# Performance work log

Hardware: AMD Instinct MI355X
Metric: run time of the kernel (lower is better)

Reference implementation:

```python
import jax, jax.numpy as jnp
import numpy as np

SCALE = 2
GROUPS = 4


def setup_inputs() -> dict:
    key = jax.random.key(0)
    k1, k2 = jax.random.split(key, 2)
    B, C, H, W = 8, 256, 96, 96
    out_ch = 2 * GROUPS * SCALE ** 2  # 32
    x = jax.random.normal(k1, (B, C, H, W), dtype=jnp.float32)
    # offset conv: normal_init(std=0.001), bias=0
    w = jax.random.normal(k2, (out_ch, C), dtype=jnp.float32) * 0.001
    b = jnp.zeros((out_ch,), dtype=jnp.float32)
    return {"x": x, "w": w, "b": b}


def _grid_sample_bilinear_border(x, grid):
    """x: [N,C,H,W]; grid: [N,Ho,Wo,2] with (x,y) in [-1,1]; align_corners=False,
    padding_mode='border' (coords clamped to [0, size-1] before interpolation)."""
    N, C, H, W = x.shape
    Ho, Wo = grid.shape[1], grid.shape[2]
    gx = (grid[..., 0] + 1.0) * (W * 0.5) - 0.5
    gy = (grid[..., 1] + 1.0) * (H * 0.5) - 0.5
    gx = jnp.clip(gx, 0.0, W - 1.0)
    gy = jnp.clip(gy, 0.0, H - 1.0)
    x0 = jnp.floor(gx)
    y0 = jnp.floor(gy)
    wx = (gx - x0).reshape(N, 1, Ho * Wo)
    wy = (gy - y0).reshape(N, 1, Ho * Wo)
    x0i = x0.astype(jnp.int32)
    y0i = y0.astype(jnp.int32)
    x1i = jnp.minimum(x0i + 1, W - 1)
    y1i = jnp.minimum(y0i + 1, H - 1)
    xf = x.reshape(N, C, H * W)

    def gather(yi, xi):
        idx = (yi * W + xi).reshape(N, 1, Ho * Wo)
        return jnp.take_along_axis(xf, idx, axis=2)  # [N,C,Ho*Wo]

    v00 = gather(y0i, x0i)
    v01 = gather(y0i, x1i)
    v10 = gather(y1i, x0i)
    v11 = gather(y1i, x1i)
    out = (v00 * (1.0 - wx) * (1.0 - wy) + v01 * wx * (1.0 - wy)
           + v10 * (1.0 - wx) * wy + v11 * wx * wy)
    return out.reshape(N, C, Ho, Wo)


def reference(x, w, b):
    B, C, H, W = x.shape
    r, g = SCALE, GROUPS
    # 1x1 conv producing per-pixel offsets
    off = jnp.einsum('bchw,oc->bohw', x, w) + b[None, :, None, None]  # [B,32,H,W]
    Co = off.shape[1] // (r * r)  # 2*groups = 8
    # pixel_shuffle(r): out[b,c,h*r+i,w*r+j] = in[b, c*r*r + i*r + j, h, w]
    off = off.reshape(B, Co, r, r, H, W).transpose(0, 1, 4, 2, 5, 3)
    off = off.reshape(B, Co, H * r, W * r)
    off = jnp.tanh(off)
    Hs, Ws = H * r, W * r
    xr = x.reshape(B * g, C // g, H, W)
    off_field = off.reshape(B * g, 2, Hs, Ws).transpose(0, 2, 3, 1)  # [B*g,Hs,Ws,2]
    ry = jnp.linspace(-1.0 + 1.0 / Hs, 1.0 - 1.0 / Hs, Hs, dtype=jnp.float32)
    rx = jnp.linspace(-1.0 + 1.0 / Ws, 1.0 - 1.0 / Ws, Ws, dtype=jnp.float32)
    gy, gx = jnp.meshgrid(ry, rx, indexing='ij')
    base = jnp.stack([gx, gy], axis=-1)[None]  # [1,Hs,Ws,2]
    grid = base + off_field * 0.125
    out = _grid_sample_bilinear_border(xr, grid)
    return out.reshape(B, C, Hs, Ws)
```

## Files before the change

### kernel.cpp

```cpp
#include <hip/hip_runtime.h>

#define Cc  256
#define Hh  96
#define Ww  96
#define HW  (Hh*Ww)
#define OC  32
#define HS  192
#define WSS 192
#define PLANE (HS*WSS)
#define WT_FLOATS (Cc*OC)

__global__ __launch_bounds__(256) void transpose_w_kernel(
    const float* __restrict__ w, float* __restrict__ wt)
{
    const int l = blockIdx.x * 256 + threadIdx.x;
    const int o = l >> 8, c = l & 255;
    wt[c * OC + o] = w[l];
}

__global__ __launch_bounds__(256) void conv_offset_kernel(
    const float* __restrict__ x, const float* __restrict__ wt,
    const float* __restrict__ bias, float* __restrict__ grid_buf)
{
    __shared__ float lds[Cc * OC];
    const int tid   = threadIdx.x;
    const int pix   = tid & 63;
    const int slice = __builtin_amdgcn_readfirstlane(threadIdx.x >> 6);

    const int p  = blockIdx.x * 64 + pix;
    const int b  = p / HW;
    const int hw = p - b * HW;
    const float* xp = x + (size_t)b * Cc * HW + (size_t)(slice * 64) * HW + hw;
    const float* wp = wt + slice * (64 * OC);

    float acc[OC];
    #pragma unroll
    for (int o = 0; o < OC; ++o) acc[o] = 0.0f;

    #pragma unroll 4
    for (int c = 0; c < 64; ++c) {
        float xv = xp[(size_t)c * HW];
        const float4* w4 = (const float4*)&wp[c * OC];
        #pragma unroll
        for (int o4 = 0; o4 < 8; ++o4) {
            float4 wv = w4[o4];
            acc[4*o4+0] = fmaf(wv.x, xv, acc[4*o4+0]);
            acc[4*o4+1] = fmaf(wv.y, xv, acc[4*o4+1]);
            acc[4*o4+2] = fmaf(wv.z, xv, acc[4*o4+2]);
            acc[4*o4+3] = fmaf(wv.w, xv, acc[4*o4+3]);
        }
    }

    #pragma unroll
    for (int o = 0; o < OC; ++o) lds[(o * 4 + slice) * 64 + pix] = acc[o];
    __syncthreads();

    const int h  = hw / Ww;
    const int ww = hw - h * Ww;
    const int obase = slice * 8;
    #pragma unroll
    for (int oo = 0; oo < 8; ++oo) {
        const int o = obase + oo;
        float s = lds[(o * 4 + 0) * 64 + pix]
                + lds[(o * 4 + 1) * 64 + pix]
                + lds[(o * 4 + 2) * 64 + pix]
                + lds[(o * 4 + 3) * 64 + pix] + bias[o];
        const int co  = o >> 2;
        const int rem = o & 3;
        const int i   = rem >> 1;
        const int j   = rem & 1;
        const int gr  = co >> 1;
        const int k   = co & 1;
        const int hs  = 2 * h + i;
        const int ws  = 2 * ww + j;
        float t = tanhf(s);
        float coord = (k == 0) ? (0.5f * (float)ws - 0.25f + 6.0f * t)
                               : (0.5f * (float)hs - 0.25f + 6.0f * t);
        coord = fminf(fmaxf(coord, 0.0f), 95.0f);
        const int bg = b * 4 + gr;
        grid_buf[(((size_t)bg * HS + hs) * WSS + ws) * 2 + k] = coord;
    }
}

__global__ __launch_bounds__(512) void sample_kernel(
    const float* __restrict__ x, const float* __restrict__ grid_buf,
    float* __restrict__ out)
{
    __shared__ __align__(16) float2 pl[9344];
    const int bp  = blockIdx.x;
    const int b   = bp >> 7;
    const int c2  = (bp & 127) << 1;
    const int bg  = b * 4 + (c2 >> 6);
    const int tid = threadIdx.x;

    const float4* xp0 = (const float4*)(x + (size_t)(b * 256 + c2) * HW);
    const float4* xp1 = (const float4*)(x + (size_t)(b * 256 + c2 + 1) * HW);
    float4* pl4 = (float4*)pl;
    #pragma unroll
    for (int i = 0; i < 5; ++i) {
        int t = tid + 512 * i;
        if (i < 4 || t < 2304) {
            float4 a = xp0[t];
            float4 bb = xp1[t];
            pl4[2 * t]     = make_float4(a.x, bb.x, a.y, bb.y);
            pl4[2 * t + 1] = make_float4(a.z, bb.z, a.w, bb.w);
        }
    }
    if (tid < 128) pl[9216 + tid] = make_float2(0.0f, 0.0f);
    __syncthreads();

    const float* gbase = grid_buf + (size_t)bg * PLANE * 2;
    float* ob0 = out + (size_t)(b * 256 + c2) * PLANE;
    float* ob1 = ob0 + PLANE;

    #pragma unroll 2
    for (int r = 0; r < 72; ++r) {
        const int idx = r * 512 + tid;
        float2 g = *(const float2*)(gbase + (size_t)idx * 2);
        float x0f = floorf(g.x), y0f = floorf(g.y);
        float wx = g.x - x0f, wy = g.y - y0f;
        int base = (int)fmaf(y0f, 96.0f, x0f);
        float2 a0 = pl[base],      a1 = pl[base + 1];
        float2 b0 = pl[base + 96], b1 = pl[base + 97];
        float top0 = a0.x + (a1.x - a0.x) * wx;
        float bot0 = b0.x + (b1.x - b0.x) * wx;
        ob0[idx] = top0 + (bot0 - top0) * wy;
        float top1 = a0.y + (a1.y - a0.y) * wx;
        float bot1 = b0.y + (b1.y - b0.y) * wx;
        ob1[idx] = top1 + (bot1 - top1) * wy;
    }
}

extern "C" void kernel_launch(void* const* d_in, const int* in_sizes, int n_in,
                              void* d_out, int out_size, void* d_ws, size_t ws_size,
                              hipStream_t stream) {
    const float* x    = (const float*)d_in[0];
    const float* w    = (const float*)d_in[1];
    const float* bias = (const float*)d_in[2];
    float* out        = (float*)d_out;
    float* wt         = (float*)d_ws;
    float* grid_buf   = wt + WT_FLOATS;

    transpose_w_kernel<<<32, 256, 0, stream>>>(w, wt);
    conv_offset_kernel<<<1152, 256, 0, stream>>>(x, wt, bias, grid_buf);
    sample_kernel<<<1024, 512, 0, stream>>>(x, grid_buf, out);
}
```

Measured before the change: 388.8 us.

## Sample four channels per block with float4 LDS texels and nontemporal I/O

```diff
diff --git a/kernel.cpp b/kernel.cpp
--- a/kernel.cpp
+++ b/kernel.cpp
@@ -9,6 +9,8 @@
 #define WSS 192
 #define PLANE (HS*WSS)
 #define WT_FLOATS (Cc*OC)
+
+typedef float f32x2 __attribute__((ext_vector_type(2)));
 
 __global__ __launch_bounds__(256) void transpose_w_kernel(
     const float* __restrict__ w, float* __restrict__ wt)
@@ -37,7 +39,7 @@
     #pragma unroll
     for (int o = 0; o < OC; ++o) acc[o] = 0.0f;
 
-    #pragma unroll 4
+    #pragma unroll 8
     for (int c = 0; c < 64; ++c) {
         float xv = xp[(size_t)c * HW];
         const float4* w4 = (const float4*)&wp[c * OC];
@@ -82,52 +84,70 @@
     }
 }
 
-__global__ __launch_bounds__(512) void sample_kernel(
+__global__ __launch_bounds__(1024) void sample_kernel(
     const float* __restrict__ x, const float* __restrict__ grid_buf,
     float* __restrict__ out)
 {
-    __shared__ __align__(16) float2 pl[9344];
-    const int bp  = blockIdx.x;
-    const int b   = bp >> 7;
-    const int c2  = (bp & 127) << 1;
-    const int bg  = b * 4 + (c2 >> 6);
+    __shared__ __align__(16) float4 pl[9344];
+    const int bq  = blockIdx.x;
+    const int b   = bq >> 6;
+    const int c4  = (bq & 63) << 2;
+    const int bg  = b * 4 + (c4 >> 6);
     const int tid = threadIdx.x;
 
-    const float4* xp0 = (const float4*)(x + (size_t)(b * 256 + c2) * HW);
-    const float4* xp1 = (const float4*)(x + (size_t)(b * 256 + c2 + 1) * HW);
-    float4* pl4 = (float4*)pl;
+    const float* x0 = x + (size_t)(b * 256 + c4) * HW;
     #pragma unroll
-    for (int i = 0; i < 5; ++i) {
-        int t = tid + 512 * i;
-        if (i < 4 || t < 2304) {
-            float4 a = xp0[t];
-            float4 bb = xp1[t];
-            pl4[2 * t]     = make_float4(a.x, bb.x, a.y, bb.y);
-            pl4[2 * t + 1] = make_float4(a.z, bb.z, a.w, bb.w);
-        }
+    for (int i = 0; i < 9; ++i) {
+        int t = tid + 1024 * i;
+        float a = __builtin_nontemporal_load(x0 + t);
+        float bb = __builtin_nontemporal_load(x0 + HW + t);
+        float cc = __builtin_nontemporal_load(x0 + 2 * HW + t);
+        float dd = __builtin_nontemporal_load(x0 + 3 * HW + t);
+        pl[t] = make_float4(a, bb, cc, dd);
     }
-    if (tid < 128) pl[9216 + tid] = make_float2(0.0f, 0.0f);
+    if (tid < 128) pl[9216 + tid] = make_float4(0.f, 0.f, 0.f, 0.f);
     __syncthreads();
 
     const float* gbase = grid_buf + (size_t)bg * PLANE * 2;
-    float* ob0 = out + (size_t)(b * 256 + c2) * PLANE;
-    float* ob1 = ob0 + PLANE;
+    float* ob = out + (size_t)(b * 256 + c4) * PLANE;
 
     #pragma unroll 2
-    for (int r = 0; r < 72; ++r) {
-        const int idx = r * 512 + tid;
-        float2 g = *(const float2*)(gbase + (size_t)idx * 2);
-        float x0f = floorf(g.x), y0f = floorf(g.y);
-        float wx = g.x - x0f, wy = g.y - y0f;
-        int base = (int)fmaf(y0f, 96.0f, x0f);
-        float2 a0 = pl[base],      a1 = pl[base + 1];
-        float2 b0 = pl[base + 96], b1 = pl[base + 97];
-        float top0 = a0.x + (a1.x - a0.x) * wx;
-        float bot0 = b0.x + (b1.x - b0.x) * wx;
-        ob0[idx] = top0 + (bot0 - top0) * wy;
-        float top1 = a0.y + (a1.y - a0.y) * wx;
-        float bot1 = b0.y + (b1.y - b0.y) * wx;
-        ob1[idx] = top1 + (bot1 - top1) * wy;
+    for (int r = 0; r < 18; ++r) {
+        const int idx = r * 2048 + tid * 2;
+        float4 g = *(const float4*)(gbase + (size_t)idx * 2);
+        float4 r0, r1;
+        {
+            float x0f = floorf(g.x), y0f = floorf(g.y);
+            float wx = g.x - x0f, wy = g.y - y0f;
+            int base = (int)fmaf(y0f, 96.0f, x0f);
+            float4 a0 = pl[base],      a1 = pl[base + 1];
+            float4 b0 = pl[base + 96], b1 = pl[base + 97];
+            float tx, bx;
+            tx = a0.x + (a1.x - a0.x) * wx; bx = b0.x + (b1.x - b0.x) * wx; r0.x = tx + (bx - tx) * wy;
+            tx = a0.y + (a1.y - a0.y) * wx; bx = b0.y + (b1.y - b0.y) * wx; r0.y = tx + (bx - tx) * wy;
+            tx = a0.z + (a1.z - a0.z) * wx; bx = b0.z + (b1.z - b0.z) * wx; r0.z = tx + (bx - tx) * wy;
+            tx = a0.w + (a1.w - a0.w) * wx; bx = b0.w + (b1.w - b0.w) * wx; r0.w = tx + (bx - tx) * wy;
+        }
+        {
+            float x0f = floorf(g.z), y0f = floorf(g.w);
+            float wx = g.z - x0f, wy = g.w - y0f;
+            int base = (int)fmaf(y0f, 96.0f, x0f);
+            float4 a0 = pl[base],      a1 = pl[base + 1];
+            float4 b0 = pl[base + 96], b1 = pl[base + 97];
+            float tx, bx;
+            tx = a0.x + (a1.x - a0.x) * wx; bx = b0.x + (b1.x - b0.x) * wx; r1.x = tx + (bx - tx) * wy;
+            tx = a0.y + (a1.y - a0.y) * wx; bx = b0.y + (b1.y - b0.y) * wx; r1.y = tx + (bx - tx) * wy;
+            tx = a0.z + (a1.z - a0.z) * wx; bx = b0.z + (b1.z - b0.z) * wx; r1.z = tx + (bx - tx) * wy;
+            tx = a0.w + (a1.w - a0.w) * wx; bx = b0.w + (b1.w - b0.w) * wx; r1.w = tx + (bx - tx) * wy;
+        }
+        f32x2 s0 = {r0.x, r1.x};
+        f32x2 s1 = {r0.y, r1.y};
+        f32x2 s2 = {r0.z, r1.z};
+        f32x2 s3 = {r0.w, r1.w};
+        __builtin_nontemporal_store(s0, (f32x2*)(ob + idx));
+        __builtin_nontemporal_store(s1, (f32x2*)(ob + PLANE + idx));
+        __builtin_nontemporal_store(s2, (f32x2*)(ob + 2 * PLANE + idx));
+        __builtin_nontemporal_store(s3, (f32x2*)(ob + 3 * PLANE + idx));
     }
 }
 
@@ -143,5 +163,5 @@
 
     transpose_w_kernel<<<32, 256, 0, stream>>>(w, wt);
     conv_offset_kernel<<<1152, 256, 0, stream>>>(x, wt, bias, grid_buf);
-    sample_kernel<<<1024, 512, 0, stream>>>(x, grid_buf, out);
+    sample_kernel<<<512, 1024, 0, stream>>>(x, grid_buf, out);
 }
```

Measured after the change: 382.2 us. No clear change (-1.7%).
